# Kernel optimization log

Hardware: AMD Instinct MI355X
Metric: run time of the kernel (lower is better)

The kernel has to match this reference:

```python
import jax, jax.numpy as jnp
import numpy as np

D_MODEL = 768
D_FF = 3072
N_BEHAVIORS = 4
EPS = 1e-12


def layer_norm(x, g, b):
    m = jnp.mean(x, axis=-1, keepdims=True)
    v = jnp.mean(jnp.square(x - m), axis=-1, keepdims=True)
    return (x - m) * jax.lax.rsqrt(v + EPS) * g + b


def setup_inputs() -> dict:
    key = jax.random.key(0)
    ks = jax.random.split(key, 8)
    B, L = 8, 2048
    s1 = 1.0 / np.sqrt(D_MODEL)
    s2 = 1.0 / np.sqrt(D_FF)
    return {
        "input_tensor": jax.random.normal(ks[0], (B, L, D_MODEL), dtype=jnp.float32),
        "type_seq": jax.random.randint(ks[1], (B, L), 0, N_BEHAVIORS + 1),
        # per-behavior FeedForward params, stacked on leading n dim
        "W1": jax.random.normal(ks[2], (N_BEHAVIORS, D_MODEL, D_FF), dtype=jnp.float32) * s1,
        "b1": jnp.zeros((N_BEHAVIORS, D_FF), dtype=jnp.float32),
        "W2": jax.random.normal(ks[3], (N_BEHAVIORS, D_FF, D_MODEL), dtype=jnp.float32) * s2,
        "b2": jnp.zeros((N_BEHAVIORS, D_MODEL), dtype=jnp.float32),
        "ln_g": jnp.ones((N_BEHAVIORS, D_MODEL), dtype=jnp.float32),
        "ln_b": jnp.zeros((N_BEHAVIORS, D_MODEL), dtype=jnp.float32),
        # outer LayerNorm params
        "out_g": jnp.ones((D_MODEL,), dtype=jnp.float32),
        "out_b": jnp.zeros((D_MODEL,), dtype=jnp.float32),
    }


def reference(input_tensor, type_seq, W1, b1, W2, b2, ln_g, ln_b, out_g, out_b):
    n = W1.shape[0]
    # run every behavior's FeedForward over the full sequence (dense over-compute)
    h = jnp.einsum('BLH,nHF->nBLF', input_tensor, W1) + b1[:, None, None, :]
    h = jax.nn.gelu(h, approximate=False)  # torch 'gelu' = exact erf form
    h = jnp.einsum('nBLF,nFH->nBLH', h, W2) + b2[:, None, None, :]
    # per-expert residual LayerNorm (FeedForward with residual=True)
    h = layer_norm(h + input_tensor[None], ln_g[:, None, None, :], ln_b[:, None, None, :])
    # prepend zeros branch (class 0 = padding) then one-hot select per token
    stacked = jnp.concatenate([jnp.zeros_like(input_tensor)[None], h], axis=0)  # [n+1,B,L,H]
    onehot = jax.nn.one_hot(type_seq, n + 1, dtype=input_tensor.dtype)  # [B,L,n+1]
    sel = jnp.einsum('nBLH,BLn->BLH', stacked, onehot)
    # dropout is identity in eval; fused residual + LayerNorm
    return layer_norm(sel + input_tensor, out_g, out_b)
```

## Files before the change

kernel.cpp:

```cpp
#include <hip/hip_runtime.h>
#include <hip/hip_bf16.h>
#include <math.h>

#define NTOK   16384
#define DM     768
#define DF     3072
#define NEXP   4

#define RBLKS  64
#define XBLKS  768
#define WBLKS  288
#define PREP_BLKS (RBLKS + XBLKS + WBLKS)
#define W2BLKS 288

typedef short bf16x8 __attribute__((ext_vector_type(8)));
typedef float f32x4  __attribute__((ext_vector_type(4)));

#define WS_CNT    0u
#define WS_BASES  256u
#define WS_POS    512u
#define WS_LIST   (512u + 65536u)
#define WS_XB     (WS_LIST + 262144u)
#define WS_W1T    (WS_XB + 25165824u)
#define WS_W2T    (WS_W1T + 18874368u)
#define WS_H1     (WS_W2T + 18874368u)
#define WS_H2     (WS_H1 + 100663296u)
#define WS_END    (WS_H2 + 25165824u)

__device__ __forceinline__ ushort f2bf(float f) {
    unsigned int v; __builtin_memcpy(&v, &f, 4);
    v = v + 0x7fffu + ((v >> 16) & 1u);
    return (ushort)(v >> 16);
}
__device__ __forceinline__ float bf2f(ushort u) {
    unsigned int v = ((unsigned int)u) << 16;
    float f; __builtin_memcpy(&f, &v, 4); return f;
}

__device__ __forceinline__ float fast_gelu(float v) {
    float y = v + 0.044715f * v * v * v;
    float e = __builtin_amdgcn_exp2f(-2.3022082f * y);
    return v * __builtin_amdgcn_rcpf(1.0f + e);
}

typedef __attribute__((address_space(1))) const void gvoid_t;
typedef __attribute__((address_space(3))) void lvoid_t;
__device__ __forceinline__ void cp16(const void* g, void* l) {
    __builtin_amdgcn_global_load_lds((gvoid_t*)g, (lvoid_t*)l, 16, 0, 0);
}

__device__ __forceinline__ int xcd_remap(int id, int T) {
    const int q = T >> 3, r = T & 7;
    const int x = id & 7, j = id >> 3;
    return (x < r ? x * (q + 1) : r * (q + 1) + (x - r) * q) + j;
}

__global__ __launch_bounds__(256) void prep_kernel(
    const int* __restrict__ type_seq, const float* __restrict__ X,
    const float* __restrict__ W1,
    int* __restrict__ cnt,
    int* __restrict__ pos_of, int* __restrict__ list,
    ushort* __restrict__ Xb, ushort* __restrict__ W1t) {
    __shared__ ushort tbuf[2][64 * 72];
    __shared__ int lcnt[NEXP];
    __shared__ int lbase[NEXP];
    const int tid = threadIdx.x;
    const int bid = blockIdx.x;

    if (bid < RBLKS) {
        if (tid < NEXP) lcnt[tid] = 0;
        __syncthreads();
        const int lane = tid & 63;
        const int t = bid * 256 + tid;
        const int k = type_seq[t];
        int my_e = -1, my_p = 0;
#pragma unroll
        for (int e = 0; e < NEXP; ++e) {
            unsigned long long m = __ballot(k == e + 1);
            int total = __popcll(m);
            int b = 0;
            if (lane == 0 && total) b = atomicAdd(&lcnt[e], total);
            b = __shfl(b, 0, 64);
            if (k == e + 1) {
                my_e = e;
                my_p = b + __popcll(m & ((1ull << lane) - 1ull));
            }
        }
        __syncthreads();
        if (tid < NEXP && lcnt[tid] > 0)
            lbase[tid] = atomicAdd(&cnt[tid], lcnt[tid]);
        __syncthreads();
        if (my_e >= 0) {
            int gp = lbase[my_e] + my_p;
            list[my_e * NTOK + gp] = t;
            pos_of[t] = gp;
        }
        return;
    }

    int id = bid - RBLKS;
    if (id < XBLKS) {
        size_t ibase = ((size_t)id * 8 * 256 + tid) * 8;
        float4 va[8], vb[8];
#pragma unroll
        for (int k = 0; k < 8; ++k) {
            va[k] = *(const float4*)(X + ibase + (size_t)k * 2048);
            vb[k] = *(const float4*)(X + ibase + (size_t)k * 2048 + 4);
        }
#pragma unroll
        for (int k = 0; k < 8; ++k) {
            ushort tmp[8];
            tmp[0] = f2bf(va[k].x); tmp[1] = f2bf(va[k].y);
            tmp[2] = f2bf(va[k].z); tmp[3] = f2bf(va[k].w);
            tmp[4] = f2bf(vb[k].x); tmp[5] = f2bf(vb[k].y);
            tmp[6] = f2bf(vb[k].z); tmp[7] = f2bf(vb[k].w);
            *(uint4*)(Xb + ibase + (size_t)k * 2048) = *(uint4*)tmp;
        }
        return;
    }
    id -= XBLKS;
    {
        const int lr = tid >> 3;
        const int lc = (tid & 7) * 8;
        float4 v[2][2];
        const int base_tt = id * 8;
        auto LOADT = [&](int tt) {
            int z = tt / 576, rr = tt % 576, bx = rr % 48, by = rr / 48;
            const float* s0 = W1 + (size_t)z * DM * DF + (size_t)(by * 64 + lr) * DF + bx * 64 + lc;
            v[0][0] = *(const float4*)s0;       v[0][1] = *(const float4*)(s0 + 4);
            const float* s1 = s0 + (size_t)32 * DF;
            v[1][0] = *(const float4*)s1;       v[1][1] = *(const float4*)(s1 + 4);
        };
        LOADT(base_tt);
#pragma unroll 1
        for (int k = 0; k < 8; ++k) {
            ushort* tb = &tbuf[k & 1][0];
#pragma unroll
            for (int q = 0; q < 2; ++q) {
                int r = lr + q * 32;
                ushort tmp[8];
                tmp[0] = f2bf(v[q][0].x); tmp[1] = f2bf(v[q][0].y);
                tmp[2] = f2bf(v[q][0].z); tmp[3] = f2bf(v[q][0].w);
                tmp[4] = f2bf(v[q][1].x); tmp[5] = f2bf(v[q][1].y);
                tmp[6] = f2bf(v[q][1].z); tmp[7] = f2bf(v[q][1].w);
                int sw = (((lc >> 3) ^ ((r >> 3) & 7)) << 3);
                *(uint4*)&tb[r * 72 + sw] = *(uint4*)tmp;
            }
            if (k < 7) LOADT(base_tt + k + 1);
            __syncthreads();
            int tt = base_tt + k;
            int z = tt / 576, rr = tt % 576, bx = rr % 48, by = rr / 48;
#pragma unroll
            for (int q = 0; q < 2; ++q) {
                int r = lr + q * 32;
                ushort tmp[8];
#pragma unroll
                for (int j = 0; j < 8; ++j)
                    tmp[j] = tb[(lc + j) * 72 +
                                ((((r >> 3) & 7) ^ (((lc + j) >> 3) & 7)) << 3) + (r & 7)];
                *(uint4*)(W1t + (size_t)z * DM * DF + (size_t)(bx * 64 + r) * DM + by * 64 + lc) = *(uint4*)tmp;
            }
        }
    }
}

__global__ __launch_bounds__(512, 4) void gemm1_kernel(
    const ushort* __restrict__ Xb, const ushort* __restrict__ W1t,
    const float* __restrict__ b1, const int* __restrict__ cnt,
    const int* __restrict__ list, ushort* __restrict__ h1,
    const float* __restrict__ W2, ushort* __restrict__ W2t) {
    __shared__ __align__(16) short As[3][4096];
    __shared__ __align__(16) short Bs[3][4096];
    const int tid = threadIdx.x;

    const int c0 = cnt[0], c1 = cnt[1], c2 = cnt[2], c3 = cnt[3];
    const int p0 = (c0 + 127) >> 7, p1 = (c1 + 127) >> 7, p2 = (c2 + 127) >> 7;
    const int mb = p0 + p1 + p2 + ((c3 + 127) >> 7);
    const int T = mb * 24;
    int id = blockIdx.y * 24 + blockIdx.x;

    if (id >= T) {
        int wid = id - T;
        if (wid >= W2BLKS) return;
        ushort* tb = (ushort*)&As[0][0];
        const int lr = tid >> 3;
        const int lc = (tid & 7) * 8;
#pragma unroll 1
        for (int k = 0; k < 8; ++k) {
            int tt = wid * 8 + k;
            int zz = tt / 576, rr = tt % 576, bx = rr % 12, by = rr / 12;
            size_t mbase = (size_t)zz * DM * DF;
            const float* s = W2 + mbase + (size_t)(by * 64 + lr) * DM + bx * 64 + lc;
            float4 v0 = *(const float4*)s;
            float4 v1 = *(const float4*)(s + 4);
            ushort tmp[8];
            tmp[0] = f2bf(v0.x); tmp[1] = f2bf(v0.y); tmp[2] = f2bf(v0.z); tmp[3] = f2bf(v0.w);
            tmp[4] = f2bf(v1.x); tmp[5] = f2bf(v1.y); tmp[6] = f2bf(v1.z); tmp[7] = f2bf(v1.w);
            int sw = (((lc >> 3) ^ ((lr >> 3) & 7)) << 3);
            __syncthreads();
            *(uint4*)&tb[lr * 72 + sw] = *(uint4*)tmp;
            __syncthreads();
            ushort o[8];
#pragma unroll
            for (int j = 0; j < 8; ++j)
                o[j] = tb[(lc + j) * 72 +
                          ((((lr >> 3) & 7) ^ (((lc + j) >> 3) & 7)) << 3) + (lr & 7)];
            *(uint4*)(W2t + mbase + (size_t)(bx * 64 + lr) * DF + by * 64 + lc) = *(uint4*)o;
        }
        return;
    }

    id = xcd_remap(id, T);
    const int y = id / 24;
    const int n0 = (id % 24) * 128;
    const int q1 = p0, q2 = p0 + p1, q3 = p0 + p1 + p2;
    const int e = (y >= q1) + (y >= q2) + (y >= q3);
    const int mstart = (e > 0) * p0 + (e > 1) * p1 + (e > 2) * p2;
    const int m0 = (y - mstart) << 7;
    const int count = (e == 0) ? c0 : ((e == 1) ? c1 : ((e == 2) ? c2 : c3));
    const int base = (e > 0) * c0 + (e > 1) * c1 + (e > 2) * c2;
    const int NK = DM / 32;

    const int wave = tid >> 6, lane = tid & 63;
    const int wm = (wave & 1) * 64, wn = (wave >> 1) * 32;
    const int lrow = lane & 15;
    const int qg = lane >> 4;

    int r0 = min(m0 + (tid >> 2), count - 1);
    int t0 = list[e * NTOK + r0];
    const int qsrc = ((tid & 3) ^ ((tid >> 3) & 3)) * 8;
    const ushort* a0 = Xb + (size_t)t0 * DM + qsrc;
    const ushort* Wb = W1t + (size_t)e * DF * DM;
    const ushort* bp0 = Wb + (size_t)(n0 + (tid >> 2)) * DM + qsrc;

    int aOff[4], bOff[2];
#pragma unroll
    for (int i = 0; i < 4; ++i) {
        int ra = wm + i * 16 + lrow;
        aOff[i] = ra * 32 + (qg ^ ((ra >> 1) & 3)) * 8;
    }
#pragma unroll
    for (int j = 0; j < 2; ++j) {
        int rb = wn + j * 16 + lrow;
        bOff[j] = rb * 32 + (qg ^ ((rb >> 1) & 3)) * 8;
    }

    f32x4 z = {0.f, 0.f, 0.f, 0.f};
    f32x4 acc[4][2];
#pragma unroll
    for (int i = 0; i < 4; ++i)
#pragma unroll
        for (int j = 0; j < 2; ++j) acc[i][j] = z;

    auto STAGE = [&](int wb) {
        cp16(a0, &As[0][0] + wb * 4096 + tid * 8);
        cp16(bp0, &Bs[0][0] + wb * 4096 + tid * 8);
        a0 += 32; bp0 += 32;
    };

    STAGE(0); STAGE(1);
    int rb = 0;
    for (int ks = 0; ks < NK; ++ks) {
        __builtin_amdgcn_sched_barrier(0);
        if (ks + 1 < NK) { asm volatile("s_waitcnt vmcnt(2)" ::: "memory"); }
        else             { asm volatile("s_waitcnt vmcnt(0)" ::: "memory"); }
        __builtin_amdgcn_s_barrier();
        __builtin_amdgcn_sched_barrier(0);
        if (ks + 2 < NK) {
            int wb = rb - 1; if (wb < 0) wb += 3;
            STAGE(wb);
        }
        const short* Ab = &As[0][0] + rb * 4096;
        const short* Bb = &Bs[0][0] + rb * 4096;
        bf16x8 av[4], bv[2];
#pragma unroll
        for (int i = 0; i < 4; ++i) av[i] = *(const bf16x8*)(Ab + aOff[i]);
#pragma unroll
        for (int j = 0; j < 2; ++j) bv[j] = *(const bf16x8*)(Bb + bOff[j]);
#pragma unroll
        for (int i = 0; i < 4; ++i)
#pragma unroll
            for (int j = 0; j < 2; ++j)
                acc[i][j] = __builtin_amdgcn_mfma_f32_16x16x32_bf16(av[i], bv[j], acc[i][j], 0, 0, 0);
        rb = (rb + 1 == 3) ? 0 : rb + 1;
    }

    float bias[2];
#pragma unroll
    for (int nt = 0; nt < 2; ++nt)
        bias[nt] = b1[e * DF + n0 + wn + nt * 16 + lrow];
#pragma unroll
    for (int mt = 0; mt < 4; ++mt) {
        int gm = m0 + wm + mt * 16 + (lane >> 4) * 4;
#pragma unroll
        for (int nt = 0; nt < 2; ++nt) {
            int gn = n0 + wn + nt * 16 + lrow;
#pragma unroll
            for (int r = 0; r < 4; ++r) {
                int i = gm + r;
                if (i < count) {
                    float v = acc[mt][nt][r] + bias[nt];
                    h1[(size_t)(base + i) * DF + gn] = f2bf(fast_gelu(v));
                }
            }
        }
    }
}

__global__ __launch_bounds__(256, 3) void gemm2_kernel(
    const ushort* __restrict__ h1, const ushort* __restrict__ W2t,
    const float* __restrict__ b2, const int* __restrict__ cnt,
    ushort* __restrict__ h2) {
    const int c0 = cnt[0], c1 = cnt[1], c2 = cnt[2], c3 = cnt[3];
    const int p0 = (c0 + 127) >> 7, p1 = (c1 + 127) >> 7, p2 = (c2 + 127) >> 7;
    const int mb = p0 + p1 + p2 + ((c3 + 127) >> 7);
    const int T = mb * 6;
    int id = blockIdx.y * 6 + blockIdx.x;
    if (id >= T) return;
    id = xcd_remap(id, T);
    const int y = id / 6;
    const int n0 = (id % 6) * 128;
    const int q1 = p0, q2 = p0 + p1, q3 = p0 + p1 + p2;
    const int e = (y >= q1) + (y >= q2) + (y >= q3);
    const int mstart = (e > 0) * p0 + (e > 1) * p1 + (e > 2) * p2;
    const int m0 = (y - mstart) << 7;
    const int count = (e == 0) ? c0 : ((e == 1) ? c1 : ((e == 2) ? c2 : c3));
    const int base = (e > 0) * c0 + (e > 1) * c1 + (e > 2) * c2;
    const int NK = DF / 32;

    __shared__ __align__(16) short As[3][4096];
    __shared__ __align__(16) short Bs[3][4096];

    const int tid = threadIdx.x;
    const int wave = tid >> 6, lane = tid & 63;
    const int wm = (wave & 1) * 64, wn = (wave >> 1) * 64;
    const int lrow = lane & 15;
    const int qg = lane >> 4;

    const int srow = tid >> 2;
    const int qsrc = ((tid & 3) ^ ((tid >> 3) & 3)) * 8;
    int r0 = min(m0 + srow, count - 1);
    int r1 = min(m0 + 64 + srow, count - 1);
    const ushort* a0 = h1 + (size_t)(base + r0) * DF + qsrc;
    const ushort* a1 = h1 + (size_t)(base + r1) * DF + qsrc;
    const ushort* Wb = W2t + (size_t)e * DM * DF;
    const ushort* bp0 = Wb + (size_t)(n0 + srow) * DF + qsrc;
    const ushort* bp1 = bp0 + (size_t)64 * DF;

    int aOff[4], bOff[4];
#pragma unroll
    for (int i = 0; i < 4; ++i) {
        int ra = wm + i * 16 + lrow;
        aOff[i] = ra * 32 + (qg ^ ((ra >> 1) & 3)) * 8;
        int rbo = wn + i * 16 + lrow;
        bOff[i] = rbo * 32 + (qg ^ ((rbo >> 1) & 3)) * 8;
    }

    f32x4 z = {0.f, 0.f, 0.f, 0.f};
    f32x4 acc[4][4];
#pragma unroll
    for (int i = 0; i < 4; ++i)
#pragma unroll
        for (int j = 0; j < 4; ++j) acc[i][j] = z;

    auto STAGE = [&](int wb) {
        cp16(a0, &As[wb][0] + tid * 8);
        cp16(a1, &As[wb][2048] + tid * 8);
        cp16(bp0, &Bs[wb][0] + tid * 8);
        cp16(bp1, &Bs[wb][2048] + tid * 8);
        a0 += 32; a1 += 32; bp0 += 32; bp1 += 32;
    };

    STAGE(0); STAGE(1);
    int rb = 0;
    for (int ks = 0; ks < NK; ++ks) {
        __builtin_amdgcn_sched_barrier(0);
        if (ks + 1 < NK) { asm volatile("s_waitcnt vmcnt(4)" ::: "memory"); }
        else             { asm volatile("s_waitcnt vmcnt(0)" ::: "memory"); }
        __builtin_amdgcn_s_barrier();
        __builtin_amdgcn_sched_barrier(0);
        if (ks + 2 < NK) {
            int wb = rb - 1; if (wb < 0) wb += 3;
            STAGE(wb);
        }
        const short* Ab = &As[rb][0];
        const short* Bb = &Bs[rb][0];
        bf16x8 av[4], bv[4];
#pragma unroll
        for (int i = 0; i < 4; ++i) av[i] = *(const bf16x8*)(Ab + aOff[i]);
#pragma unroll
        for (int j = 0; j < 4; ++j) bv[j] = *(const bf16x8*)(Bb + bOff[j]);
#pragma unroll
        for (int i = 0; i < 4; ++i)
#pragma unroll
            for (int j = 0; j < 4; ++j)
                acc[i][j] = __builtin_amdgcn_mfma_f32_16x16x32_bf16(av[i], bv[j], acc[i][j], 0, 0, 0);
        rb = (rb + 1 == 3) ? 0 : rb + 1;
    }

    float bias[4];
#pragma unroll
    for (int j = 0; j < 4; ++j)
        bias[j] = b2[e * DM + n0 + wn + j * 16 + lrow];
#pragma unroll
    for (int i = 0; i < 4; ++i) {
        int gm = m0 + wm + i * 16 + qg * 4;
#pragma unroll
        for (int j = 0; j < 4; ++j) {
            int gn = n0 + wn + j * 16 + lrow;
#pragma unroll
            for (int r = 0; r < 4; ++r) {
                int row = gm + r;
                if (row < count)
                    h2[(size_t)(base + row) * DM + gn] = f2bf(acc[i][j][r] + bias[j]);
            }
        }
    }
}

__global__ __launch_bounds__(256) void finalize_kernel(
    const float* __restrict__ X, const int* __restrict__ type_seq,
    const int* __restrict__ pos_of, const int* __restrict__ cnt,
    const ushort* __restrict__ h2,
    const float* __restrict__ ln_g, const float* __restrict__ ln_b,
    const float* __restrict__ out_g, const float* __restrict__ out_b,
    float* __restrict__ out) {
    const int tid = threadIdx.x;
    const int wave = tid >> 6, lane = tid & 63;
    const int col0 = lane * 4;
    const int c0 = cnt[0], c1 = cnt[1], c2 = cnt[2];

#pragma unroll 1
    for (int ti = 0; ti < 4; ++ti) {
        const int t = blockIdx.x * 16 + wave * 4 + ti;
        const int k = type_seq[t];

        const float* Xr = X + (size_t)t * DM;
        float4 xv[3];
#pragma unroll
        for (int j = 0; j < 3; ++j) xv[j] = *(const float4*)(Xr + col0 + j * 256);

        float rv[12];
        if (k > 0) {
            const int e = k - 1;
            const int base = (e > 0) * c0 + (e > 1) * c1 + (e > 2) * c2;
            const size_t row = (size_t)(base + pos_of[t]);
            const ushort* hr = h2 + row * DM;
            float v[12];
            float s1 = 0.f, s2 = 0.f;
#pragma unroll
            for (int j = 0; j < 3; ++j) {
                ushort4 hv = *(const ushort4*)(hr + col0 + j * 256);
                float f0 = bf2f(hv.x) + xv[j].x;
                float f1 = bf2f(hv.y) + xv[j].y;
                float f2 = bf2f(hv.z) + xv[j].z;
                float f3 = bf2f(hv.w) + xv[j].w;
                v[j * 4 + 0] = f0; v[j * 4 + 1] = f1;
                v[j * 4 + 2] = f2; v[j * 4 + 3] = f3;
                s1 += (f0 + f1) + (f2 + f3);
                s2 += (f0 * f0 + f1 * f1) + (f2 * f2 + f3 * f3);
            }
#pragma unroll
            for (int off = 32; off > 0; off >>= 1) {
                s1 += __shfl_xor(s1, off, 64);
                s2 += __shfl_xor(s2, off, 64);
            }
            float m = s1 * (1.f / DM);
            float inv = rsqrtf(s2 * (1.f / DM) - m * m + 1e-12f);
#pragma unroll
            for (int j = 0; j < 3; ++j) {
                float4 g = *(const float4*)(ln_g + e * DM + col0 + j * 256);
                float4 b = *(const float4*)(ln_b + e * DM + col0 + j * 256);
                rv[j * 4 + 0] = (v[j * 4 + 0] - m) * inv * g.x + b.x;
                rv[j * 4 + 1] = (v[j * 4 + 1] - m) * inv * g.y + b.y;
                rv[j * 4 + 2] = (v[j * 4 + 2] - m) * inv * g.z + b.z;
                rv[j * 4 + 3] = (v[j * 4 + 3] - m) * inv * g.w + b.w;
            }
        } else {
#pragma unroll
            for (int j = 0; j < 12; ++j) rv[j] = 0.f;
        }

        float w[12];
        float s1 = 0.f, s2 = 0.f;
#pragma unroll
        for (int j = 0; j < 3; ++j) {
            float f0 = rv[j * 4 + 0] + xv[j].x;
            float f1 = rv[j * 4 + 1] + xv[j].y;
            float f2 = rv[j * 4 + 2] + xv[j].z;
            float f3 = rv[j * 4 + 3] + xv[j].w;
            w[j * 4 + 0] = f0; w[j * 4 + 1] = f1;
            w[j * 4 + 2] = f2; w[j * 4 + 3] = f3;
            s1 += (f0 + f1) + (f2 + f3);
            s2 += (f0 * f0 + f1 * f1) + (f2 * f2 + f3 * f3);
        }
#pragma unroll
        for (int off = 32; off > 0; off >>= 1) {
            s1 += __shfl_xor(s1, off, 64);
            s2 += __shfl_xor(s2, off, 64);
        }
        float m = s1 * (1.f / DM);
        float inv = rsqrtf(s2 * (1.f / DM) - m * m + 1e-12f);
#pragma unroll
        for (int j = 0; j < 3; ++j) {
            float4 g = *(const float4*)(out_g + col0 + j * 256);
            float4 b = *(const float4*)(out_b + col0 + j * 256);
            float4 o;
            o.x = (w[j * 4 + 0] - m) * inv * g.x + b.x;
            o.y = (w[j * 4 + 1] - m) * inv * g.y + b.y;
            o.z = (w[j * 4 + 2] - m) * inv * g.z + b.z;
            o.w = (w[j * 4 + 3] - m) * inv * g.w + b.w;
            *(float4*)(out + (size_t)t * DM + col0 + j * 256) = o;
        }
    }
}

extern "C" void kernel_launch(void* const* d_in, const int* in_sizes, int n_in,
                              void* d_out, int out_size, void* d_ws, size_t ws_size,
                              hipStream_t stream) {
    if (ws_size < (size_t)WS_END) return;

    const float* X     = (const float*)d_in[0];
    const int*   type  = (const int*)d_in[1];
    const float* W1    = (const float*)d_in[2];
    const float* b1    = (const float*)d_in[3];
    const float* W2    = (const float*)d_in[4];
    const float* b2    = (const float*)d_in[5];
    const float* ln_g  = (const float*)d_in[6];
    const float* ln_b  = (const float*)d_in[7];
    const float* out_g = (const float*)d_in[8];
    const float* out_b = (const float*)d_in[9];
    float* out = (float*)d_out;

    char* ws = (char*)d_ws;
    int* cnt    = (int*)(ws + WS_CNT);
    int* pos_of = (int*)(ws + WS_POS);
    int* list   = (int*)(ws + WS_LIST);
    ushort* Xb  = (ushort*)(ws + WS_XB);
    ushort* W1t = (ushort*)(ws + WS_W1T);
    ushort* W2t = (ushort*)(ws + WS_W2T);
    ushort* h1  = (ushort*)(ws + WS_H1);
    ushort* h2  = (ushort*)(ws + WS_H2);

    hipMemsetAsync(cnt, 0, NEXP * sizeof(int), stream);
    prep_kernel<<<PREP_BLKS, 256, 0, stream>>>(type, X, W1,
                                               cnt, pos_of, list, Xb, W1t);
    gemm1_kernel<<<dim3(24, 144), 512, 0, stream>>>(Xb, W1t, b1, cnt, list, h1, W2, W2t);
    gemm2_kernel<<<dim3(6, 132), 256, 0, stream>>>(h1, W2t, b2, cnt, h2);
    finalize_kernel<<<NTOK / 16, 256, 0, stream>>>(X, type, pos_of, cnt, h2, ln_g, ln_b, out_g, out_b, out);
}
```

Measured before the change: 373.4 us.

## Enlarge gemm2 tiles to 256x128 with 512 threads and BK=64 split MFMA phases

Restructures the second grouped GEMM so each block computes a 256x128 output tile with 8 waves instead of 128x128 with 4 waves, and doubles the K step to 64. The goal is more reuse of each W2 tile, fewer barriers per unit of work, and fewer blocks. The loop now issues loads earlier, uses finer vmcnt waits, splits the MFMA work into two phases separated by barriers, and raises wave priority with setprio during MFMA. In exchange, shared memory grows to about 144 KB per block, which lowers occupancy, and padding waste grows on experts whose token count is not a multiple of 256.

```diff
diff --git a/kernel.cpp b/kernel.cpp
--- a/kernel.cpp
+++ b/kernel.cpp
@@ -307,13 +307,13 @@
     }
 }
 
-__global__ __launch_bounds__(256, 3) void gemm2_kernel(
+__global__ __launch_bounds__(512, 2) void gemm2_kernel(
     const ushort* __restrict__ h1, const ushort* __restrict__ W2t,
     const float* __restrict__ b2, const int* __restrict__ cnt,
     ushort* __restrict__ h2) {
     const int c0 = cnt[0], c1 = cnt[1], c2 = cnt[2], c3 = cnt[3];
-    const int p0 = (c0 + 127) >> 7, p1 = (c1 + 127) >> 7, p2 = (c2 + 127) >> 7;
-    const int mb = p0 + p1 + p2 + ((c3 + 127) >> 7);
+    const int p0 = (c0 + 255) >> 8, p1 = (c1 + 255) >> 8, p2 = (c2 + 255) >> 8;
+    const int mb = p0 + p1 + p2 + ((c3 + 255) >> 8);
     const int T = mb * 6;
     int id = blockIdx.y * 6 + blockIdx.x;
     if (id >= T) return;
@@ -323,37 +323,41 @@
     const int q1 = p0, q2 = p0 + p1, q3 = p0 + p1 + p2;
     const int e = (y >= q1) + (y >= q2) + (y >= q3);
     const int mstart = (e > 0) * p0 + (e > 1) * p1 + (e > 2) * p2;
-    const int m0 = (y - mstart) << 7;
+    const int m0 = (y - mstart) << 8;
     const int count = (e == 0) ? c0 : ((e == 1) ? c1 : ((e == 2) ? c2 : c3));
     const int base = (e > 0) * c0 + (e > 1) * c1 + (e > 2) * c2;
-    const int NK = DF / 32;
-
-    __shared__ __align__(16) short As[3][4096];
-    __shared__ __align__(16) short Bs[3][4096];
+    const int NK = DF / 64;
+
+    __shared__ __align__(16) short As[3][16384];
+    __shared__ __align__(16) short Bs[3][8192];
 
     const int tid = threadIdx.x;
     const int wave = tid >> 6, lane = tid & 63;
-    const int wm = (wave & 1) * 64, wn = (wave >> 1) * 64;
+    const int wr = wave >> 1, wc = wave & 1;
     const int lrow = lane & 15;
     const int qg = lane >> 4;
 
-    const int srow = tid >> 2;
-    const int qsrc = ((tid & 3) ^ ((tid >> 3) & 3)) * 8;
-    int r0 = min(m0 + srow, count - 1);
-    int r1 = min(m0 + 64 + srow, count - 1);
-    const ushort* a0 = h1 + (size_t)(base + r0) * DF + qsrc;
-    const ushort* a1 = h1 + (size_t)(base + r1) * DF + qsrc;
+    const int srow = tid >> 3;
+    const int qsrc = ((tid & 7) ^ (srow & 7)) * 8;
+    const ushort* aP[4];
+#pragma unroll
+    for (int s = 0; s < 4; ++s) {
+        int r = min(m0 + srow + s * 64, count - 1);
+        aP[s] = h1 + (size_t)(base + r) * DF + qsrc;
+    }
     const ushort* Wb = W2t + (size_t)e * DM * DF;
-    const ushort* bp0 = Wb + (size_t)(n0 + srow) * DF + qsrc;
-    const ushort* bp1 = bp0 + (size_t)64 * DF;
+    const ushort* bP[2];
+#pragma unroll
+    for (int s = 0; s < 2; ++s)
+        bP[s] = Wb + (size_t)(n0 + srow + s * 64) * DF + qsrc;
 
     int aOff[4], bOff[4];
 #pragma unroll
     for (int i = 0; i < 4; ++i) {
-        int ra = wm + i * 16 + lrow;
-        aOff[i] = ra * 32 + (qg ^ ((ra >> 1) & 3)) * 8;
-        int rbo = wn + i * 16 + lrow;
-        bOff[i] = rbo * 32 + (qg ^ ((rbo >> 1) & 3)) * 8;
+        int ra = wr * 64 + i * 16 + lrow;
+        aOff[i] = ra * 64 + (qg ^ (ra & 7)) * 8;
+        int rb = wc * 64 + i * 16 + lrow;
+        bOff[i] = rb * 64 + (qg ^ (rb & 7)) * 8;
     }
 
     f32x4 z = {0.f, 0.f, 0.f, 0.f};
@@ -363,51 +367,88 @@
 #pragma unroll
         for (int j = 0; j < 4; ++j) acc[i][j] = z;
 
-    auto STAGE = [&](int wb) {
-        cp16(a0, &As[wb][0] + tid * 8);
-        cp16(a1, &As[wb][2048] + tid * 8);
-        cp16(bp0, &Bs[wb][0] + tid * 8);
-        cp16(bp1, &Bs[wb][2048] + tid * 8);
-        a0 += 32; a1 += 32; bp0 += 32; bp1 += 32;
+    auto STAGE = [&](int buf) {
+        short* aD = &As[buf][0] + tid * 8;
+        short* bD = &Bs[buf][0] + tid * 8;
+#pragma unroll
+        for (int s = 0; s < 4; ++s) { cp16(aP[s], aD + s * 4096); aP[s] += 64; }
+#pragma unroll
+        for (int s = 0; s < 2; ++s) { cp16(bP[s], bD + s * 4096); bP[s] += 64; }
     };
 
     STAGE(0); STAGE(1);
-    int rb = 0;
-    for (int ks = 0; ks < NK; ++ks) {
+    int rb = 0, sb = 2;
+    for (int kt = 0; kt < NK; ++kt) {
+        if (kt + 2 < NK) {
+            STAGE(sb);
+            sb = (sb + 1 == 3) ? 0 : sb + 1;
+        }
         __builtin_amdgcn_sched_barrier(0);
-        if (ks + 1 < NK) { asm volatile("s_waitcnt vmcnt(4)" ::: "memory"); }
-        else             { asm volatile("s_waitcnt vmcnt(0)" ::: "memory"); }
+        if (kt + 2 < NK)      { asm volatile("s_waitcnt vmcnt(12)" ::: "memory"); }
+        else if (kt + 1 < NK) { asm volatile("s_waitcnt vmcnt(6)" ::: "memory"); }
+        else                  { asm volatile("s_waitcnt vmcnt(0)" ::: "memory"); }
         __builtin_amdgcn_s_barrier();
         __builtin_amdgcn_sched_barrier(0);
-        if (ks + 2 < NK) {
-            int wb = rb - 1; if (wb < 0) wb += 3;
-            STAGE(wb);
-        }
+
         const short* Ab = &As[rb][0];
         const short* Bb = &Bs[rb][0];
-        bf16x8 av[4], bv[4];
-#pragma unroll
-        for (int i = 0; i < 4; ++i) av[i] = *(const bf16x8*)(Ab + aOff[i]);
-#pragma unroll
-        for (int j = 0; j < 4; ++j) bv[j] = *(const bf16x8*)(Bb + bOff[j]);
-#pragma unroll
-        for (int i = 0; i < 4; ++i)
-#pragma unroll
-            for (int j = 0; j < 4; ++j)
-                acc[i][j] = __builtin_amdgcn_mfma_f32_16x16x32_bf16(av[i], bv[j], acc[i][j], 0, 0, 0);
+
+        bf16x8 av0[2][2], bv[4][2];
+#pragma unroll
+        for (int i = 0; i < 2; ++i) {
+            av0[i][0] = *(const bf16x8*)(Ab + aOff[i]);
+            av0[i][1] = *(const bf16x8*)(Ab + (aOff[i] ^ 32));
+        }
+#pragma unroll
+        for (int j = 0; j < 4; ++j) {
+            bv[j][0] = *(const bf16x8*)(Bb + bOff[j]);
+            bv[j][1] = *(const bf16x8*)(Bb + (bOff[j] ^ 32));
+        }
+        asm volatile("s_waitcnt lgkmcnt(0)" ::: "memory");
+        __builtin_amdgcn_sched_barrier(0);
+        __builtin_amdgcn_s_setprio(1);
+#pragma unroll
+        for (int i = 0; i < 2; ++i)
+#pragma unroll
+            for (int j = 0; j < 4; ++j) {
+                acc[i][j] = __builtin_amdgcn_mfma_f32_16x16x32_bf16(av0[i][0], bv[j][0], acc[i][j], 0, 0, 0);
+                acc[i][j] = __builtin_amdgcn_mfma_f32_16x16x32_bf16(av0[i][1], bv[j][1], acc[i][j], 0, 0, 0);
+            }
+        __builtin_amdgcn_s_setprio(0);
+        __builtin_amdgcn_s_barrier();
+
+        bf16x8 av1[2][2];
+#pragma unroll
+        for (int i = 0; i < 2; ++i) {
+            av1[i][0] = *(const bf16x8*)(Ab + aOff[2 + i]);
+            av1[i][1] = *(const bf16x8*)(Ab + (aOff[2 + i] ^ 32));
+        }
+        asm volatile("s_waitcnt lgkmcnt(0)" ::: "memory");
+        __builtin_amdgcn_sched_barrier(0);
+        __builtin_amdgcn_s_setprio(1);
+#pragma unroll
+        for (int i = 0; i < 2; ++i)
+#pragma unroll
+            for (int j = 0; j < 4; ++j) {
+                acc[2 + i][j] = __builtin_amdgcn_mfma_f32_16x16x32_bf16(av1[i][0], bv[j][0], acc[2 + i][j], 0, 0, 0);
+                acc[2 + i][j] = __builtin_amdgcn_mfma_f32_16x16x32_bf16(av1[i][1], bv[j][1], acc[2 + i][j], 0, 0, 0);
+            }
+        __builtin_amdgcn_s_setprio(0);
+        __builtin_amdgcn_s_barrier();
+
         rb = (rb + 1 == 3) ? 0 : rb + 1;
     }
 
     float bias[4];
 #pragma unroll
     for (int j = 0; j < 4; ++j)
-        bias[j] = b2[e * DM + n0 + wn + j * 16 + lrow];
+        bias[j] = b2[e * DM + n0 + wc * 64 + j * 16 + lrow];
 #pragma unroll
     for (int i = 0; i < 4; ++i) {
-        int gm = m0 + wm + i * 16 + qg * 4;
+        int gm = m0 + wr * 64 + i * 16 + qg * 4;
 #pragma unroll
         for (int j = 0; j < 4; ++j) {
-            int gn = n0 + wn + j * 16 + lrow;
+            int gn = n0 + wc * 64 + j * 16 + lrow;
 #pragma unroll
             for (int r = 0; r < 4; ++r) {
                 int row = gm + r;
@@ -546,6 +587,6 @@
     prep_kernel<<<PREP_BLKS, 256, 0, stream>>>(type, X, W1,
                                                cnt, pos_of, list, Xb, W1t);
     gemm1_kernel<<<dim3(24, 144), 512, 0, stream>>>(Xb, W1t, b1, cnt, list, h1, W2, W2t);
-    gemm2_kernel<<<dim3(6, 132), 256, 0, stream>>>(h1, W2t, b2, cnt, h2);
+    gemm2_kernel<<<dim3(6, 68), 512, 0, stream>>>(h1, W2t, b2, cnt, h2);
     finalize_kernel<<<NTOK / 16, 256, 0, stream>>>(X, type, pos_of, cnt, h2, ln_g, ln_b, out_g, out_b, out);
 }
```

Measured after the change: 422.2 us. 1.13x slower.
